# Kernel optimization log

Measured on AMD Instinct MI355X. Metric: run time of the kernel, lower is better.

Reference implementation:

```python
import jax, jax.numpy as jnp
import numpy as np

R_MAX = 32
S_MAX = 2
C_Z = 128
NTB = 2 * R_MAX + 2 + 1  # num_tok_pos_bins = 67
IN_DIM = 2 * NTB + (2 * S_MAX + 2) + 1  # 141


def _compute_bins(asym_id, entity_id, residue_index, token_index, sym_id, mask):
    # Pairwise [B, N, N] bucket indices, matching the torch module exactly.
    same_chain = asym_id[..., :, None] == asym_id[..., None, :]
    same_entity = entity_id[..., :, None] == entity_id[..., None, :]
    d_res = jnp.where(
        same_chain,
        jnp.clip(residue_index[..., :, None] - residue_index[..., None, :] + R_MAX, 0, 2 * R_MAX),
        2 * R_MAX + 1,
    )
    same_res = residue_index[..., :, None] == residue_index[..., None, :]
    tok_dist = token_index[..., :, None] - token_index[..., None, :] + R_MAX
    d_tok = jnp.where(same_chain & same_res, jnp.clip(tok_dist, 0, 2 * R_MAX), 2 * R_MAX + 1)
    d_chain = jnp.where(
        same_entity,
        jnp.clip(sym_id[..., :, None] - sym_id[..., None, :] + S_MAX, 0, 2 * S_MAX),
        2 * S_MAX + 1,
    )
    # index-removal spoofing: masked pairs go to the last token-position bin
    d_tok = jnp.where(mask, NTB - 1, d_tok)
    d_res = jnp.where(mask, NTB - 1, d_res)
    return d_res, d_tok, same_entity, d_chain


def setup_inputs() -> dict:
    key = jax.random.key(0)
    ks = jax.random.split(key, 7)
    B, N = 1, 768
    asym_id = jax.random.randint(ks[0], (B, N), 0, 4, dtype=jnp.int32)
    entity_id = jax.random.randint(ks[1], (B, N), 0, 3, dtype=jnp.int32)
    residue_index = jnp.sort(jax.random.randint(ks[2], (B, N), 0, 200, dtype=jnp.int32), axis=-1)
    token_index = jnp.sort(jax.random.randint(ks[3], (B, N), 0, 300, dtype=jnp.int32), axis=-1)
    sym_id = jax.random.randint(ks[4], (B, N), 0, 4, dtype=jnp.int32)
    unindexing_pair_mask = jax.random.randint(ks[5], (B, N, N), 0, 2) > 0
    W = jax.random.normal(ks[6], (IN_DIM, C_Z), dtype=jnp.float32) * 0.02
    return {
        "asym_id": asym_id,
        "entity_id": entity_id,
        "residue_index": residue_index,
        "token_index": token_index,
        "sym_id": sym_id,
        "unindexing_pair_mask": unindexing_pair_mask,
        "W": W,
    }


def reference(asym_id, entity_id, residue_index, token_index, sym_id, unindexing_pair_mask, W):
    d_res, d_tok, same_entity, d_chain = _compute_bins(
        asym_id, entity_id, residue_index, token_index, sym_id, unindexing_pair_mask
    )
    # linear(one_hot concat) == gather-sum of weight row blocks (same math, fused):
    # concat layout: [relpos (NTB) | reltoken (NTB) | same_entity (1) | relchain (2*S_MAX+2)]
    W_res = W[:NTB]                      # [67, c_z]
    W_tok = W[NTB:2 * NTB]               # [67, c_z]
    w_ent = W[2 * NTB]                   # [c_z]
    W_chain = W[2 * NTB + 1:]            # [6, c_z]
    out = (
        W_res[d_res]
        + W_tok[d_tok]
        + same_entity.astype(W.dtype)[..., None] * w_ent
        + W_chain[d_chain]
    )  # [B, N, N, c_z]
    return out
```

## Files before the change

### kernel.cpp

```cpp
#include <hip/hip_runtime.h>

#define R_MAX 32
#define S_MAX 2
#define C_Z   128
#define NTB   (2 * R_MAX + 2 + 1)
#define IN_DIM (2 * NTB + (2 * S_MAX + 2) + 1)
#define JT   256

__device__ __forceinline__ int clampi(int x, int lo, int hi) {
    return min(max(x, lo), hi);
}

__global__ __launch_bounds__(256) void relpos_kernel(
    const int* __restrict__ asym_id,
    const int* __restrict__ entity_id,
    const int* __restrict__ residue_index,
    const int* __restrict__ token_index,
    const int* __restrict__ sym_id,
    const int* __restrict__ mask,
    const float* __restrict__ W,
    float* __restrict__ out,
    int N)
{
    __shared__ int code_s[JT];

    const int tid = threadIdx.x;
    const int row = blockIdx.y;
    const int jb  = blockIdx.x * JT;
    const int b   = row / N;

    const int ai = asym_id[row];
    const int ei = entity_id[row];
    const int ri = residue_index[row];
    const int ti = token_index[row];
    const int si = sym_id[row];

    {
        int j = jb + tid;
        int code = 0;
        if (j < N) {
            int jrow = b * N + j;
            int aj = asym_id[jrow];
            int ej = entity_id[jrow];
            int rj = residue_index[jrow];
            int tj = token_index[jrow];
            int sj = sym_id[jrow];

            bool same_chain  = (ai == aj);
            bool same_entity = (ei == ej);
            bool same_res    = (ri == rj);

            int d_res   = same_chain ? clampi(ri - rj + R_MAX, 0, 2 * R_MAX) : (2 * R_MAX + 1);
            int d_tok   = (same_chain && same_res) ? clampi(ti - tj + R_MAX, 0, 2 * R_MAX)
                                                   : (2 * R_MAX + 1);
            int d_chain = same_entity ? clampi(si - sj + S_MAX, 0, 2 * S_MAX) : (2 * S_MAX + 1);

            if (mask[(long long)row * N + j] != 0) { d_res = NTB - 1; d_tok = NTB - 1; }

            code = d_res | (d_tok << 7) | (d_chain << 14) | (same_entity ? (1 << 17) : 0);
        }
        code_s[tid] = code;
    }
    __syncthreads();

    const int chunk = tid & 31;
    const int psub  = tid >> 5;
    const float4* __restrict__ W4 = (const float4*)W;

    const float4 e = W4[(2 * NTB) * 32 + chunk];

    float4* __restrict__ outp = (float4*)out + ((long long)row * N + jb) * 32;
    const int jmax = min(JT, N - jb);

    #pragma unroll 4
    for (int it = 0; it < JT / 8; ++it) {
        int pair = it * 8 + psub;
        if (pair >= jmax) break;
        int code = code_s[pair];

        int d_res   = code & 127;
        int d_tok   = (code >> 7) & 127;
        int d_chain = (code >> 14) & 7;
        float se    = (code >> 17) ? 1.0f : 0.0f;

        float4 r = W4[d_res * 32 + chunk];
        float4 t = W4[(NTB + d_tok) * 32 + chunk];
        float4 c = W4[(2 * NTB + 1 + d_chain) * 32 + chunk];

        float4 o;
        o.x = r.x + t.x + se * e.x + c.x;
        o.y = r.y + t.y + se * e.y + c.y;
        o.z = r.z + t.z + se * e.z + c.z;
        o.w = r.w + t.w + se * e.w + c.w;

        outp[(long long)pair * 32 + chunk] = o;
    }
}

extern "C" void kernel_launch(void* const* d_in, const int* in_sizes, int n_in,
                              void* d_out, int out_size, void* d_ws, size_t ws_size,
                              hipStream_t stream) {
    const int*   asym_id       = (const int*)d_in[0];
    const int*   entity_id     = (const int*)d_in[1];
    const int*   residue_index = (const int*)d_in[2];
    const int*   token_index   = (const int*)d_in[3];
    const int*   sym_id        = (const int*)d_in[4];
    const int*   mask          = (const int*)d_in[5];
    const float* W             = (const float*)d_in[6];
    float*       out           = (float*)d_out;

    long long BN      = in_sizes[0];
    long long mask_sz = in_sizes[5];
    int N = (int)(mask_sz / BN);

    dim3 grid((unsigned)((N + JT - 1) / JT), (unsigned)BN);
    dim3 block(256);

    relpos_kernel<<<grid, block, 0, stream>>>(
        asym_id, entity_id, residue_index, token_index, sym_id,
        mask, W, out, N);
}
```

Measured before the change: 361.4 us.

## Transpose code tile into registers, fully unroll, and use nontemporal output stores

Stores pair codes in a transposed shared layout so each thread loads all its 32 codes with vector LDS reads into registers. The gather-sum loop is fully unrolled, with a fast path for full tiles, and output stores become nontemporal to avoid polluting caches with the large write-only output. Address arithmetic is simplified by folding the chunk offset into the base pointers. This raises register use and code size.

```diff
diff --git a/kernel.cpp b/kernel.cpp
--- a/kernel.cpp
+++ b/kernel.cpp
@@ -6,6 +6,8 @@
 #define NTB   (2 * R_MAX + 2 + 1)
 #define IN_DIM (2 * NTB + (2 * S_MAX + 2) + 1)
 #define JT   256
+
+typedef float vf4 __attribute__((ext_vector_type(4)));
 
 __device__ __forceinline__ int clampi(int x, int lo, int hi) {
     return min(max(x, lo), hi);
@@ -22,7 +24,7 @@
     float* __restrict__ out,
     int N)
 {
-    __shared__ int code_s[JT];
+    __shared__ int codeT[JT];
 
     const int tid = threadIdx.x;
     const int row = blockIdx.y;
@@ -59,42 +61,61 @@
 
             code = d_res | (d_tok << 7) | (d_chain << 14) | (same_entity ? (1 << 17) : 0);
         }
-        code_s[tid] = code;
+        codeT[(tid & 7) * 32 + (tid >> 3)] = code;
     }
     __syncthreads();
 
     const int chunk = tid & 31;
     const int psub  = tid >> 5;
-    const float4* __restrict__ W4 = (const float4*)W;
+    const vf4* __restrict__ W4 = (const vf4*)W + chunk;
 
-    const float4 e = W4[(2 * NTB) * 32 + chunk];
+    const vf4 e = W4[(2 * NTB) * 32];
 
-    float4* __restrict__ outp = (float4*)out + ((long long)row * N + jb) * 32;
+    vf4* __restrict__ outp = (vf4*)out + ((long long)row * N + jb) * 32 + chunk;
     const int jmax = min(JT, N - jb);
 
-    #pragma unroll 4
-    for (int it = 0; it < JT / 8; ++it) {
-        int pair = it * 8 + psub;
-        if (pair >= jmax) break;
-        int code = code_s[pair];
+    int4 creg[8];
+    {
+        const int4* cp = (const int4*)&codeT[psub * 32];
+        #pragma unroll
+        for (int k = 0; k < 8; ++k) creg[k] = cp[k];
+    }
 
-        int d_res   = code & 127;
-        int d_tok   = (code >> 7) & 127;
-        int d_chain = (code >> 14) & 7;
-        float se    = (code >> 17) ? 1.0f : 0.0f;
+#define PROC(codev, itv)                                                      \
+    {                                                                         \
+        int code    = (codev);                                                \
+        int pair    = (itv) * 8 + psub;                                       \
+        int d_res   = code & 127;                                             \
+        int d_tok   = (code >> 7) & 127;                                      \
+        int d_chain = (code >> 14) & 7;                                       \
+        float se    = (float)((code >> 17) & 1);                              \
+        vf4 r  = W4[d_res * 32];                                              \
+        vf4 t  = W4[(NTB + d_tok) * 32];                                      \
+        vf4 cc = W4[(2 * NTB + 1 + d_chain) * 32];                            \
+        vf4 o  = r + t + se * e + cc;                                         \
+        __builtin_nontemporal_store(o, &outp[pair * 32]);                     \
+    }
 
-        float4 r = W4[d_res * 32 + chunk];
-        float4 t = W4[(NTB + d_tok) * 32 + chunk];
-        float4 c = W4[(2 * NTB + 1 + d_chain) * 32 + chunk];
-
-        float4 o;
-        o.x = r.x + t.x + se * e.x + c.x;
-        o.y = r.y + t.y + se * e.y + c.y;
-        o.z = r.z + t.z + se * e.z + c.z;
-        o.w = r.w + t.w + se * e.w + c.w;
-
-        outp[(long long)pair * 32 + chunk] = o;
+    if (jmax == JT) {
+        #pragma unroll
+        for (int k = 0; k < 8; ++k) {
+            int4 c = creg[k];
+            PROC(c.x, 4 * k + 0)
+            PROC(c.y, 4 * k + 1)
+            PROC(c.z, 4 * k + 2)
+            PROC(c.w, 4 * k + 3)
+        }
+    } else {
+        #pragma unroll
+        for (int k = 0; k < 8; ++k) {
+            int4 c = creg[k];
+            if (4 * k * 8 + psub < jmax)       PROC(c.x, 4 * k + 0)
+            if ((4 * k + 1) * 8 + psub < jmax) PROC(c.y, 4 * k + 1)
+            if ((4 * k + 2) * 8 + psub < jmax) PROC(c.z, 4 * k + 2)
+            if ((4 * k + 3) * 8 + psub < jmax) PROC(c.w, 4 * k + 3)
+        }
     }
+#undef PROC
 }
 
 extern "C" void kernel_launch(void* const* d_in, const int* in_sizes, int n_in,
```

Result: faster. 319.8 us (-11.5%).
